# Performance work log

Hardware: AMD Instinct MI355X
Metric: run time of the kernel (lower is better)

Reference implementation:

```python
import jax, jax.numpy as jnp
import numpy as np

B, S, D = 4, 4096, 256

def setup_inputs() -> dict:
    key = jax.random.key(0)
    kx, kq, kk, kv = jax.random.split(key, 4)
    # torch nn.Linear(D, D) weight init: U(-1/sqrt(D), 1/sqrt(D)), stored as [out, in]
    bound = 1.0 / np.sqrt(D)
    x = jax.random.normal(kx, (B, S, D), dtype=jnp.float32)
    Wq = jax.random.uniform(kq, (D, D), dtype=jnp.float32, minval=-bound, maxval=bound)
    Wk = jax.random.uniform(kk, (D, D), dtype=jnp.float32, minval=-bound, maxval=bound)
    Wv = jax.random.uniform(kv, (D, D), dtype=jnp.float32, minval=-bound, maxval=bound)
    return {"x": x, "Wq": Wq, "Wk": Wk, "Wv": Wv}

def reference(x, Wq, Wk, Wv):
    # Linear with weight [out,in]: y = x @ W^T
    Q = jnp.einsum('bsd,ed->bse', x, Wq)
    K = jnp.einsum('bsd,ed->bse', x, Wk)
    V = jnp.einsum('bsd,ed->bse', x, Wv)
    d = x.shape[-1]
    scores = jnp.einsum('bqe,bke->bqk', Q, K) / jnp.sqrt(jnp.float32(d))  # [B,S,S]
    S_len = x.shape[1]
    causal = jnp.tril(jnp.ones((S_len, S_len), dtype=bool))
    scores = jnp.where(causal, scores, -jnp.inf)
    attn = jax.nn.softmax(scores, axis=-1)
    return jnp.einsum('bqk,bke->bqe', attn, V)
```

## Files before the change

kernel.cpp:

```cpp
#include <hip/hip_runtime.h>

typedef unsigned short u16;
typedef unsigned int u32;
typedef __attribute__((ext_vector_type(8))) short bf16x8;
typedef __attribute__((ext_vector_type(4))) float f32x4;
typedef __attribute__((ext_vector_type(16))) float f32x16;
typedef __attribute__((ext_vector_type(2))) unsigned int u32x2;

#define MFMA16 __builtin_amdgcn_mfma_f32_16x16x32_bf16
#define MFMA32 __builtin_amdgcn_mfma_f32_32x32x16_bf16

__device__ __forceinline__ u16 f2bf(float f) {
  u32 u = __builtin_bit_cast(u32, f);
  u = u + 0x7FFFu + ((u >> 16) & 1u);
  return (u16)(u >> 16);
}
__device__ __forceinline__ u32 pk2(float lo, float hi) {
  return (u32)f2bf(lo) | ((u32)f2bf(hi) << 16);
}
__device__ __forceinline__ float bf2f(u32 x) {
  return __builtin_bit_cast(float, x << 16);
}
__device__ __forceinline__ u32 cvtpk(float lo, float hi) {
  u32 r;
  asm("v_cvt_pk_bf16_f32 %0, %1, %2" : "=v"(r) : "v"(lo), "v"(hi));
  return r;
}
__device__ __forceinline__ void pswap(u32& x, u32& y) {
  asm("v_permlane32_swap_b32 %0, %1" : "+v"(x), "+v"(y));
}
__device__ __forceinline__ void gld16(const void* gp, void* lp) {
  __builtin_amdgcn_global_load_lds((const __attribute__((address_space(1))) u32*)gp,
                                   (__attribute__((address_space(3))) u32*)lp, 16, 0, 0);
}

__global__ __launch_bounds__(256) void cvt_kernel(
    const float* __restrict__ wq, const float* __restrict__ wk,
    const float* __restrict__ wv, u16* __restrict__ wbf) {
  int idx = blockIdx.x * 256 + threadIdx.x;
  const float* W = (idx < 16384) ? wq : (idx < 32768) ? wk : wv;
  int k = idx & 16383;
  float4 v = ((const float4*)W)[k];
  uint2 u; u.x = pk2(v.x, v.y); u.y = pk2(v.z, v.w);
  ((uint2*)wbf)[idx] = u;
}

__global__ __launch_bounds__(256, 2) void proj_kernel(
    const float* __restrict__ x, const u16* __restrict__ wbf,
    u16* __restrict__ Qs, u16* __restrict__ Ks, u16* __restrict__ Vt) {
  int tile = blockIdx.x, mat = blockIdx.y;
  int tid = threadIdx.x, w = tid >> 6, lane = tid & 63, b15 = lane & 15, g = lane >> 4;
  int base = tile * 64 + w * 16;
  const u16* W = wbf + mat * 65536;
  const float* Xp = x + (size_t)(base + b15) * 256;
  f32x4 acc[16] = {};
#pragma unroll
  for (int kk = 0; kk < 8; ++kk) {
    float4 xa = *(const float4*)(Xp + kk * 32 + g * 8);
    float4 xb = *(const float4*)(Xp + kk * 32 + g * 8 + 4);
    union { u32 u[4]; bf16x8 v; } xu;
    xu.u[0] = cvtpk(xa.x, xa.y); xu.u[1] = cvtpk(xa.z, xa.w);
    xu.u[2] = cvtpk(xb.x, xb.y); xu.u[3] = cvtpk(xb.z, xb.w);
    bf16x8 xf = xu.v;
    if (mat < 2) {
#pragma unroll
      for (int eb = 0; eb < 16; ++eb) {
        bf16x8 wf = *(const bf16x8*)(W + (size_t)(eb * 16 + b15) * 256 + kk * 32 + g * 8);
        acc[eb] = MFMA16(xf, wf, acc[eb], 0, 0, 0);
      }
    } else {
#pragma unroll
      for (int eb = 0; eb < 16; ++eb) {
        bf16x8 wf = *(const bf16x8*)(W + (size_t)(eb * 16 + b15) * 256 + kk * 32 + g * 8);
        acc[eb] = MFMA16(wf, xf, acc[eb], 0, 0, 0);
      }
    }
  }
  if (mat < 2) {
    float scale = (mat == 0) ? 0.0901684400555602f : 1.0f;
    u16* dst = (mat == 0) ? Qs : Ks;
#pragma unroll
    for (int eb = 0; eb < 16; ++eb)
#pragma unroll
      for (int r = 0; r < 4; ++r)
        dst[(size_t)(base + g * 4 + r) * 256 + eb * 16 + b15] = f2bf(acc[eb][r] * scale);
  } else {
    int sglob = base + b15;
    int b = sglob >> 12, sl = sglob & 4095;
#pragma unroll
    for (int eb = 0; eb < 16; ++eb)
#pragma unroll
      for (int r = 0; r < 4; ++r) {
        int e = eb * 16 + g * 4 + r;
        Vt[((size_t)(b * 256 + e) << 12) + sl] = f2bf(acc[eb][r]);
      }
  }
}

__global__ __launch_bounds__(256, 2) void attn_kernel(
    const u16* __restrict__ Qs, const u16* __restrict__ Ks_,
    const u16* __restrict__ Vt_, u16* __restrict__ pacc, float2* __restrict__ pml) {
  __shared__ u16 Kd[2][8192];
  __shared__ u16 Vd[2][8192];

  int bid = blockIdx.x;
  int xcd = bid & 7;
  int b = xcd >> 1;
  int j = ((bid >> 3) << 1) | (bid & 1);
  int t0, c0, t1 = -1, c1 = 0;
  if (j < 16) {
    int g = j & 7;
    if (j < 8) { t0 = 4 * g;     t1 = 4 * g + 3; }
    else       { t0 = 4 * g + 1; t1 = 4 * g + 2; }
    c0 = g; c1 = g;
  } else {
    int jj = j - 16;
    int g = 1;
#pragma unroll
    for (int gg = 2; gg <= 7; ++gg) if (jj >= 2 * gg * (gg - 1)) g = gg;
    int r = jj - 2 * g * (g - 1);
    t0 = 4 * g + r / g; c0 = r % g;
  }

  int tid = threadIdx.x, w = tid >> 6, lane = tid & 63;
  int l31 = lane & 31, h = lane >> 5;

  int Koff[4], Voff[4];
#pragma unroll
  for (int i = 0; i < 4; ++i) {
    int o = (w * 4 + i) * 1024 + lane * 16;
    int row = o >> 9;
    Koff[i] = row * 512 + ((o & 511) ^ ((row & 15) << 4));
    int e = o >> 6;
    Voff[i] = e * 8192 + ((o & 63) ^ (((e >> 1) & 3) << 4));
  }
  const char* Kgb = (const char*)(Ks_ + (size_t)b * 4096 * 256);
  const char* Vgb = (const char*)(Vt_ + (size_t)b * 1048576);
  char* KL = (char*)&Kd[0][0];
  char* VL = (char*)&Vd[0][0];

  auto stage = [&](int buf, int kt) {
    size_t kb = (size_t)kt * 32 * 512;
    size_t vb = (size_t)kt * 64;
#pragma unroll
    for (int i = 0; i < 4; ++i)
      gld16(Kgb + kb + Koff[i], KL + buf * 16384 + (w * 4 + i) * 1024);
#pragma unroll
    for (int i = 0; i < 4; ++i)
      gld16(Vgb + vb + Voff[i], VL + buf * 16384 + (w * 4 + i) * 1024);
  };

  auto process = [&](int tt, int c) {
    int g4 = tt >> 2;
    int uid = b * 144 + 2 * g4 * (g4 + 1) + (tt & 3) * (g4 + 1) + c;
    int qbase = tt * 128 + w * 32;
    int qrow = qbase + l31;
    int kt0 = 16 * c, kt_end = min(16 * c + 16, 4 * (tt + 1));

    const u16* Qrow = Qs + ((size_t)b * 4096 + qrow) * 256;
    bf16x8 qf[16];
#pragma unroll
    for (int kc = 0; kc < 16; ++kc)
      qf[kc] = *(const bf16x8*)(Qrow + kc * 16 + h * 8);

    f32x16 acc[8] = {};
    float m0 = -3e38f, l0 = 0.f;
    stage(0, kt0);
    int cur = 0;

    for (int kt = kt0; kt < kt_end; ++kt) {
      __syncthreads();
      if (kt + 1 < kt_end) stage(cur ^ 1, kt + 1);
      int kv0 = kt * 32;
      if (kv0 <= qbase + 31) {
        const char* Kc = KL + cur * 16384;
        const char* Vc = VL + cur * 16384;
        f32x16 sA = {}, sB = {};
        __builtin_amdgcn_s_setprio(1);
#pragma unroll
        for (int kc = 0; kc < 16; kc += 2) {
          bf16x8 k0 = *(const bf16x8*)(Kc + l31 * 512 + ((kc * 32 + h * 16) ^ ((l31 & 15) << 4)));
          bf16x8 k1 = *(const bf16x8*)(Kc + l31 * 512 + (((kc + 1) * 32 + h * 16) ^ ((l31 & 15) << 4)));
          sA = MFMA32(k0, qf[kc], sA, 0, 0, 0);
          sB = MFMA32(k1, qf[kc + 1], sB, 0, 0, 0);
        }
        __builtin_amdgcn_s_setprio(0);
        f32x16 s = sA + sB;
        if (kv0 + 31 > qbase) {
#pragma unroll
          for (int r = 0; r < 16; ++r) {
            int kv = kv0 + (r & 3) + 8 * (r >> 2) + 4 * h;
            if (kv > qrow) s[r] = -3e38f;
          }
        }
        float a0 = fmaxf(fmaxf(s[0], s[1]), s[2]);
        float a1 = fmaxf(fmaxf(s[3], s[4]), s[5]);
        float a2 = fmaxf(fmaxf(s[6], s[7]), s[8]);
        float a3 = fmaxf(fmaxf(s[9], s[10]), s[11]);
        float a4 = fmaxf(fmaxf(s[12], s[13]), s[14]);
        float pmh = fmaxf(fmaxf(fmaxf(a0, a1), fmaxf(a2, a3)), fmaxf(a4, s[15]));
        if (__any(pmh > m0 + 8.f)) {
          float pm = fmaxf(pmh, __shfl_xor(pmh, 32));
          float mn = fmaxf(m0, pm);
          float sc = exp2f(m0 - mn);
          l0 *= sc;
#pragma unroll
          for (int et = 0; et < 8; ++et) acc[et] *= sc;
          m0 = mn;
        }
        float p[16];
#pragma unroll
        for (int r = 0; r < 16; ++r) p[r] = exp2f(s[r] - m0);
        u32 w0 = cvtpk(p[0], p[1]),   w1 = cvtpk(p[2], p[3]);
        u32 w2 = cvtpk(p[4], p[5]),   w3 = cvtpk(p[6], p[7]);
        u32 w4 = cvtpk(p[8], p[9]),   w5 = cvtpk(p[10], p[11]);
        u32 w6 = cvtpk(p[12], p[13]), w7 = cvtpk(p[14], p[15]);
        pswap(w0, w2); pswap(w1, w3);
        pswap(w4, w6); pswap(w5, w7);
        union { u32 uu[4]; bf16x8 vv; } pA, pB;
        pA.uu[0] = w0; pA.uu[1] = w1; pA.uu[2] = w2; pA.uu[3] = w3;
        pB.uu[0] = w4; pB.uu[1] = w5; pB.uu[2] = w6; pB.uu[3] = w7;
        __builtin_amdgcn_s_setprio(1);
#pragma unroll
        for (int et = 0; et < 8; ++et) {
          const char* vrow = Vc + (et * 32 + l31) * 64;
          int swz = ((l31 >> 1) & 3) << 4;
          bf16x8 vf0 = *(const bf16x8*)(vrow + ((h * 16) ^ swz));
          bf16x8 vf1 = *(const bf16x8*)(vrow + ((32 + h * 16) ^ swz));
          acc[et] = MFMA32(vf0, pA.vv, acc[et], 0, 0, 0);
          acc[et] = MFMA32(vf1, pB.vv, acc[et], 0, 0, 0);
        }
        __builtin_amdgcn_s_setprio(0);
        float q0 = (p[0] + p[1]) + (p[2] + p[3]);
        float q1 = (p[4] + p[5]) + (p[6] + p[7]);
        float q2 = (p[8] + p[9]) + (p[10] + p[11]);
        float q3 = (p[12] + p[13]) + (p[14] + p[15]);
        l0 += (q0 + q1) + (q2 + q3);
      }
      cur ^= 1;
    }

    l0 += __shfl_xor(l0, 32);

    u16* ppr = pacc + ((size_t)uid * 128 + w * 32 + l31) * 256;
#pragma unroll
    for (int et = 0; et < 8; ++et)
#pragma unroll
      for (int jj = 0; jj < 4; ++jj) {
        u32x2 o;
        o[0] = pk2(acc[et][4 * jj], acc[et][4 * jj + 1]);
        o[1] = pk2(acc[et][4 * jj + 2], acc[et][4 * jj + 3]);
        *(u32x2*)(ppr + et * 32 + 8 * jj + 4 * h) = o;
      }
    if (h == 0) {
      float2 a; a.x = m0; a.y = l0;
      pml[(size_t)uid * 128 + w * 32 + l31] = a;
    }
  };

  process(t0, c0);
  if (t1 >= 0) {
    __syncthreads();
    process(t1, c1);
  }
}

__global__ __launch_bounds__(256) void combine_kernel(
    const u16* __restrict__ pacc, const float2* __restrict__ pml,
    float* __restrict__ out) {
  int row = blockIdx.x * 4 + (threadIdx.x >> 6);
  int lane = threadIdx.x & 63;
  int b = row >> 12, r = row & 4095;
  int tt = r >> 7, rin = r & 127;
  int g4 = tt >> 2, nch = g4 + 1;
  int ubase = b * 144 + 2 * g4 * (g4 + 1) + (tt & 3) * (g4 + 1);
  float M = -3e38f;
  for (int cc = 0; cc < nch; ++cc)
    M = fmaxf(M, pml[(size_t)(ubase + cc) * 128 + rin].x);
  float L = 0.f, o0 = 0.f, o1 = 0.f, o2 = 0.f, o3 = 0.f;
  for (int cc = 0; cc < nch; ++cc) {
    float2 ml = pml[(size_t)(ubase + cc) * 128 + rin];
    float s = exp2f(ml.x - M);
    L += ml.y * s;
    u32x2 a = *(const u32x2*)(pacc + ((size_t)(ubase + cc) * 128 + rin) * 256 + lane * 4);
    o0 += s * bf2f(a[0] & 0xffffu); o1 += s * bf2f(a[0] >> 16);
    o2 += s * bf2f(a[1] & 0xffffu); o3 += s * bf2f(a[1] >> 16);
  }
  float inv = 1.f / L;
  f32x4 res = {o0 * inv, o1 * inv, o2 * inv, o3 * inv};
  *(f32x4*)(out + (size_t)row * 256 + lane * 4) = res;
}

extern "C" void kernel_launch(void* const* d_in, const int* in_sizes, int n_in,
                              void* d_out, int out_size, void* d_ws, size_t ws_size,
                              hipStream_t stream) {
  const float* x = (const float*)d_in[0];
  const float* wq = (const float*)d_in[1];
  const float* wk = (const float*)d_in[2];
  const float* wv = (const float*)d_in[3];
  char* ws = (char*)d_ws;
  u16* wbf = (u16*)(ws);
  u16* Qs  = (u16*)(ws + 1048576);
  u16* Ks  = (u16*)(ws + 9437184);
  u16* Vt  = (u16*)(ws + 17825792);
  u16* pacc = (u16*)(ws + 26214400);
  float2* pml = (float2*)(ws + 63963136);
  float* out = (float*)d_out;

  hipLaunchKernelGGL(cvt_kernel, dim3(192), dim3(256), 0, stream, wq, wk, wv, wbf);
  hipLaunchKernelGGL(proj_kernel, dim3(256, 3), dim3(256), 0, stream, x, wbf, Qs, Ks, Vt);
  hipLaunchKernelGGL(attn_kernel, dim3(512), dim3(256), 0, stream, Qs, Ks, Vt, pacc, pml);
  hipLaunchKernelGGL(combine_kernel, dim3(4096), dim3(256), 0, stream, pacc, pml, out);
}
```

Measured before the change: 160.0 us.

## Stage x tile in LDS once and compute Q, K, V in one block

```diff
diff --git a/kernel.cpp b/kernel.cpp
--- a/kernel.cpp
+++ b/kernel.cpp
@@ -6,6 +6,7 @@
 typedef __attribute__((ext_vector_type(4))) float f32x4;
 typedef __attribute__((ext_vector_type(16))) float f32x16;
 typedef __attribute__((ext_vector_type(2))) unsigned int u32x2;
+typedef __attribute__((ext_vector_type(4))) unsigned int u32x4;
 
 #define MFMA16 __builtin_amdgcn_mfma_f32_16x16x32_bf16
 #define MFMA32 __builtin_amdgcn_mfma_f32_32x32x16_bf16
@@ -48,52 +49,67 @@
 __global__ __launch_bounds__(256, 2) void proj_kernel(
     const float* __restrict__ x, const u16* __restrict__ wbf,
     u16* __restrict__ Qs, u16* __restrict__ Ks, u16* __restrict__ Vt) {
-  int tile = blockIdx.x, mat = blockIdx.y;
+  __shared__ u16 XL[16384];
+  int tile = blockIdx.x;
   int tid = threadIdx.x, w = tid >> 6, lane = tid & 63, b15 = lane & 15, g = lane >> 4;
-  int base = tile * 64 + w * 16;
-  const u16* W = wbf + mat * 65536;
-  const float* Xp = x + (size_t)(base + b15) * 256;
-  f32x4 acc[16] = {};
-#pragma unroll
-  for (int kk = 0; kk < 8; ++kk) {
-    float4 xa = *(const float4*)(Xp + kk * 32 + g * 8);
-    float4 xb = *(const float4*)(Xp + kk * 32 + g * 8 + 4);
-    union { u32 u[4]; bf16x8 v; } xu;
-    xu.u[0] = cvtpk(xa.x, xa.y); xu.u[1] = cvtpk(xa.z, xa.w);
-    xu.u[2] = cvtpk(xb.x, xb.y); xu.u[3] = cvtpk(xb.z, xb.w);
-    bf16x8 xf = xu.v;
-    if (mat < 2) {
-#pragma unroll
-      for (int eb = 0; eb < 16; ++eb) {
-        bf16x8 wf = *(const bf16x8*)(W + (size_t)(eb * 16 + b15) * 256 + kk * 32 + g * 8);
-        acc[eb] = MFMA16(xf, wf, acc[eb], 0, 0, 0);
-      }
-    } else {
-#pragma unroll
-      for (int eb = 0; eb < 16; ++eb) {
-        bf16x8 wf = *(const bf16x8*)(W + (size_t)(eb * 16 + b15) * 256 + kk * 32 + g * 8);
-        acc[eb] = MFMA16(wf, xf, acc[eb], 0, 0, 0);
+  int base = tile * 64;
+
+#pragma unroll
+  for (int it = 0; it < 8; ++it) {
+    int chunk = it * 256 + tid;
+    int r = chunk >> 5, cc = chunk & 31;
+    const float* xp = x + (size_t)(base + r) * 256 + cc * 8;
+    float4 xa = *(const float4*)xp, xb = *(const float4*)(xp + 4);
+    u32x4 o;
+    o[0] = cvtpk(xa.x, xa.y); o[1] = cvtpk(xa.z, xa.w);
+    o[2] = cvtpk(xb.x, xb.y); o[3] = cvtpk(xb.z, xb.w);
+    *(u32x4*)((char*)XL + r * 512 + ((cc * 16) ^ ((r & 15) << 4))) = o;
+  }
+  __syncthreads();
+
+  int xrow = w * 16 + b15;
+#pragma unroll
+  for (int mat = 0; mat < 3; ++mat) {
+    const u16* W = wbf + mat * 65536;
+    f32x4 acc[16] = {};
+#pragma unroll
+    for (int kk = 0; kk < 8; ++kk) {
+      bf16x8 xf = *(const bf16x8*)((char*)XL + xrow * 512 +
+                                   ((kk * 64 + g * 16) ^ (b15 << 4)));
+      if (mat < 2) {
+#pragma unroll
+        for (int eb = 0; eb < 16; ++eb) {
+          bf16x8 wf = *(const bf16x8*)(W + (size_t)(eb * 16 + b15) * 256 + kk * 32 + g * 8);
+          acc[eb] = MFMA16(xf, wf, acc[eb], 0, 0, 0);
+        }
+      } else {
+#pragma unroll
+        for (int eb = 0; eb < 16; ++eb) {
+          bf16x8 wf = *(const bf16x8*)(W + (size_t)(eb * 16 + b15) * 256 + kk * 32 + g * 8);
+          acc[eb] = MFMA16(wf, xf, acc[eb], 0, 0, 0);
+        }
       }
     }
-  }
-  if (mat < 2) {
-    float scale = (mat == 0) ? 0.0901684400555602f : 1.0f;
-    u16* dst = (mat == 0) ? Qs : Ks;
-#pragma unroll
-    for (int eb = 0; eb < 16; ++eb)
-#pragma unroll
-      for (int r = 0; r < 4; ++r)
-        dst[(size_t)(base + g * 4 + r) * 256 + eb * 16 + b15] = f2bf(acc[eb][r] * scale);
-  } else {
-    int sglob = base + b15;
-    int b = sglob >> 12, sl = sglob & 4095;
-#pragma unroll
-    for (int eb = 0; eb < 16; ++eb)
-#pragma unroll
-      for (int r = 0; r < 4; ++r) {
-        int e = eb * 16 + g * 4 + r;
-        Vt[((size_t)(b * 256 + e) << 12) + sl] = f2bf(acc[eb][r]);
-      }
+    if (mat < 2) {
+      float scale = (mat == 0) ? 0.0901684400555602f : 1.0f;
+      u16* dst = (mat == 0) ? Qs : Ks;
+      int srow = base + w * 16;
+#pragma unroll
+      for (int eb = 0; eb < 16; ++eb)
+#pragma unroll
+        for (int r = 0; r < 4; ++r)
+          dst[(size_t)(srow + g * 4 + r) * 256 + eb * 16 + b15] = f2bf(acc[eb][r] * scale);
+    } else {
+      int sglob = base + w * 16 + b15;
+      int b = sglob >> 12, sl = sglob & 4095;
+#pragma unroll
+      for (int eb = 0; eb < 16; ++eb)
+#pragma unroll
+        for (int r = 0; r < 4; ++r) {
+          int e = eb * 16 + g * 4 + r;
+          Vt[((size_t)(b * 256 + e) << 12) + sl] = f2bf(acc[eb][r]);
+        }
+    }
   }
 }
 
@@ -308,7 +324,7 @@
   float* out = (float*)d_out;
 
   hipLaunchKernelGGL(cvt_kernel, dim3(192), dim3(256), 0, stream, wq, wk, wv, wbf);
-  hipLaunchKernelGGL(proj_kernel, dim3(256, 3), dim3(256), 0, stream, x, wbf, Qs, Ks, Vt);
+  hipLaunchKernelGGL(proj_kernel, dim3(256), dim3(256), 0, stream, x, wbf, Qs, Ks, Vt);
   hipLaunchKernelGGL(attn_kernel, dim3(512), dim3(256), 0, stream, Qs, Ks, Vt, pacc, pml);
   hipLaunchKernelGGL(combine_kernel, dim3(4096), dim3(256), 0, stream, pacc, pml, out);
 }
```

After: 178.2 us. 1.11x slower.
